# Kernel tuning notes

Measured on AMD Instinct MI355X. Metric: run time of the kernel, lower is better.

Reference implementation:

```python
import jax, jax.numpy as jnp
import numpy as np

N = 200000
D_NODE = 256
D_EDGE = 128
D_OUT = 256
J = 17


def setup_inputs() -> dict:
    key = jax.random.key(0)
    ks = jax.random.split(key, 16)
    s = 0.02
    return {
        "nodes_1": jax.random.normal(ks[0], (N, D_NODE), jnp.float32),
        "nodes_2": jax.random.normal(ks[1], (N, D_NODE), jnp.float32),
        "edges": jax.random.normal(ks[2], (N, D_EDGE), jnp.float32),
        "node_types_1": jax.random.randint(ks[3], (N,), 0, J),
        "node_types_2": jax.random.randint(ks[4], (N,), 0, J),
        # per-joint linear stacks (torch Linear weight [out,in] stored transposed as [in,out])
        "W1": jax.random.normal(ks[5], (J, D_NODE, D_OUT), jnp.float32) * s,
        "b1": jax.random.normal(ks[6], (J, D_OUT), jnp.float32) * s,
        "W2": jax.random.normal(ks[7], (J, D_NODE, D_OUT), jnp.float32) * s,
        "b2": jax.random.normal(ks[8], (J, D_OUT), jnp.float32) * s,
        "We": jax.random.normal(ks[9], (D_EDGE, D_OUT), jnp.float32) * s,
        "be": jax.random.normal(ks[10], (D_OUT,), jnp.float32) * s,
        "Wout": jax.random.normal(ks[11], (3 * D_OUT, D_OUT), jnp.float32) * s,
        "bout": jax.random.normal(ks[12], (D_OUT,), jnp.float32) * s,
    }


def _per_type_linear(nodes, types, W, b):
    # Equivalent to: for each joint i, tmp[types==i] = nodes[types==i] @ W[i] + b[i]
    out = jnp.zeros((nodes.shape[0], W.shape[2]), nodes.dtype)
    for i in range(W.shape[0]):  # small fixed loop over joint types
        yi = nodes @ W[i] + b[i]
        out = jnp.where((types == i)[:, None], yi, out)
    return out


def reference(nodes_1, nodes_2, edges, node_types_1, node_types_2,
              W1, b1, W2, b2, We, be, Wout, bout):
    tmp_1 = _per_type_linear(nodes_1, node_types_1, W1, b1)
    tmp_2 = _per_type_linear(nodes_2, node_types_2, W2, b2)
    e = edges @ We + be
    cat = jnp.concatenate([tmp_1, tmp_2, e], axis=1)  # [N, 3*D_OUT]
    h = jax.nn.relu(cat) @ Wout + bout
    return jax.nn.relu(h)
```

## Files before the change

kernel.cpp:

```cpp
#include <hip/hip_runtime.h>


#define J_TYPES 17
#define PAIRS   (J_TYPES * J_TYPES)
#define DN      256
#define DE      128
#define DO      256
#define TILE    64
#define LDA     264
#define LDE     136

typedef short bf16x8 __attribute__((ext_vector_type(8)));
typedef float f32x4  __attribute__((ext_vector_type(4)));

#define BAR() asm volatile("s_waitcnt lgkmcnt(0)\n\ts_barrier" ::: "memory")

__device__ __forceinline__ unsigned short f2bf(float x) {
  unsigned u = __float_as_uint(x);
  return (unsigned short)((u + 0x7fffu + ((u >> 16) & 1u)) >> 16);
}

__device__ __forceinline__ unsigned cvtpk(float lo, float hi) {
  unsigned r;
  asm("v_cvt_pk_bf16_f32 %0, %1, %2" : "=v"(r) : "v"(lo), "v"(hi));
  return r;
}

__global__ void prep_w_k(const float* __restrict__ W1, const float* __restrict__ W2,
                         const float* __restrict__ We, const float* __restrict__ Wout,
                         unsigned short* __restrict__ W1t, unsigned short* __restrict__ W2t,
                         unsigned short* __restrict__ Wet, unsigned short* __restrict__ Ut) {
  const int SZW = J_TYPES * 65536;
  const int total = SZW * 2 + DE * DO + 3 * 65536;
  for (int o = blockIdx.x * blockDim.x + threadIdx.x; o < total;
       o += gridDim.x * blockDim.x) {
    int idx = o;
    if (idx < SZW) {
      int j = idx >> 16, r = idx & 65535;
      int i = r & 7, lane = (r >> 3) & 63, t = r >> 9;
      int k32 = t & 7, colt = t >> 3;
      int col = colt * 16 + (lane & 15);
      int k = k32 * 32 + ((lane >> 4) << 3) + i;
      W1t[idx] = f2bf(W1[((size_t)j * 256 + k) * 256 + col]);
    } else if ((idx -= SZW) < SZW) {
      int j = idx >> 16, r = idx & 65535;
      int i = r & 7, lane = (r >> 3) & 63, t = r >> 9;
      int k32 = t & 7, colt = t >> 3;
      int col = colt * 16 + (lane & 15);
      int k = k32 * 32 + ((lane >> 4) << 3) + i;
      W2t[idx] = f2bf(W2[((size_t)j * 256 + k) * 256 + col]);
    } else if ((idx -= SZW) < DE * DO) {
      int r = idx;
      int i = r & 7, lane = (r >> 3) & 63, t = r >> 9;
      int k32 = t & 3, colt = t >> 2;
      int col = colt * 16 + (lane & 15);
      int k = k32 * 32 + ((lane >> 4) << 3) + i;
      Wet[idx] = f2bf(We[(size_t)k * 256 + col]);
    } else {
      idx -= DE * DO;
      int p = idx >> 16, r = idx & 65535;
      int i = r & 7, lane = (r >> 3) & 63, t = r >> 9;
      int k32 = t & 7, colt = t >> 3;
      int col = colt * 16 + (lane & 15);
      int k = k32 * 32 + ((lane >> 4) << 3) + i;
      Ut[idx] = f2bf(Wout[((size_t)p * 256 + k) * 256 + col]);
    }
  }
}

__global__ void hist_k(const int* __restrict__ ty1, const int* __restrict__ ty2,
                       int* __restrict__ cnt, int N) {
  __shared__ int h[PAIRS];
  for (int i = threadIdx.x; i < PAIRS; i += blockDim.x) h[i] = 0;
  __syncthreads();
  for (int i = blockIdx.x * blockDim.x + threadIdx.x; i < N;
       i += gridDim.x * blockDim.x)
    atomicAdd(&h[ty1[i] * J_TYPES + ty2[i]], 1);
  __syncthreads();
  for (int i = threadIdx.x; i < PAIRS; i += blockDim.x) {
    int v = h[i];
    if (v) atomicAdd(&cnt[i], v);
  }
}

__global__ void scan_tiles_k(const int* __restrict__ cnt, int* __restrict__ seg,
                             int* __restrict__ tpair, int* __restrict__ tstart,
                             int* __restrict__ tnr, int* __restrict__ ntl) {
  __shared__ int s1[512], s2[512];
  int t = threadIdx.x;
  int c  = (t < PAIRS) ? cnt[t] : 0;
  int nt = (c + TILE - 1) / TILE;
  s1[t] = c; s2[t] = nt;
  __syncthreads();
  for (int o = 1; o < 512; o <<= 1) {
    int v1 = (t >= o) ? s1[t - o] : 0;
    int v2 = (t >= o) ? s2[t - o] : 0;
    __syncthreads();
    s1[t] += v1; s2[t] += v2;
    __syncthreads();
  }
  if (t < PAIRS) {
    int segstart = s1[t] - c;
    int tbase    = s2[t] - nt;
    seg[t] = segstart;
    for (int i = 0; i < nt; ++i) {
      tpair[tbase + i]  = t;
      tstart[tbase + i] = segstart + i * TILE;
      int rem = c - i * TILE;
      tnr[tbase + i] = rem < TILE ? rem : TILE;
    }
  }
  if (t == 511) ntl[0] = s2[511];
}

__global__ void scatter_k(const int* __restrict__ ty1, const int* __restrict__ ty2,
                          const int* __restrict__ seg, int* __restrict__ c2,
                          int* __restrict__ ridx, int N) {
  __shared__ int lh[PAIRS], lb[PAIRS];
  int chunk = (N + gridDim.x - 1) / gridDim.x;
  int lo = blockIdx.x * chunk;
  int hi = lo + chunk; if (hi > N) hi = N;
  for (int i = threadIdx.x; i < PAIRS; i += blockDim.x) lh[i] = 0;
  __syncthreads();
  for (int i = lo + threadIdx.x; i < hi; i += blockDim.x)
    atomicAdd(&lh[ty1[i] * J_TYPES + ty2[i]], 1);
  __syncthreads();
  for (int i = threadIdx.x; i < PAIRS; i += blockDim.x) {
    int v = lh[i];
    lb[i] = v ? atomicAdd(&c2[i], v) : 0;
    lh[i] = 0;
  }
  __syncthreads();
  for (int i = lo + threadIdx.x; i < hi; i += blockDim.x) {
    int p = ty1[i] * J_TYPES + ty2[i];
    int pos = seg[p] + lb[p] + atomicAdd(&lh[p], 1);
    ridx[pos] = i;
  }
}


__device__ __forceinline__ void stage_issue256(const float* __restrict__ src,
                                               const int* __restrict__ ridxp, int nrows,
                                               int wave, int lane, float4 f[16]) {
#pragma unroll
  for (int j = 0; j < 16; ++j) {
    int r = wave + 4 * j;
    int rc = r < nrows ? r : nrows - 1;
    int sr = ridxp[rc];
    f[j] = reinterpret_cast<const float4*>(src + (size_t)sr * DN)[lane];
  }
}

__device__ __forceinline__ void stage_write256(const float4 f[16],
                                               unsigned short* lds, int wave, int lane) {
#pragma unroll
  for (int j = 0; j < 16; ++j) {
    int r = wave + 4 * j;
    unsigned lo = cvtpk(f[j].x, f[j].y), hi = cvtpk(f[j].z, f[j].w);
    *reinterpret_cast<uint2*>(lds + r * LDA + lane * 4) = make_uint2(lo, hi);
  }
}

__device__ __forceinline__ void stage_issue128(const float* __restrict__ src,
                                               const int* __restrict__ ridxp, int nrows,
                                               int wave, int lane, float2 f[16]) {
#pragma unroll
  for (int j = 0; j < 16; ++j) {
    int r = wave + 4 * j;
    int rc = r < nrows ? r : nrows - 1;
    int sr = ridxp[rc];
    f[j] = reinterpret_cast<const float2*>(src + (size_t)sr * DE)[lane];
  }
}

__device__ __forceinline__ void stage_write128(const float2 f[16],
                                               unsigned short* lds, int wave, int lane) {
#pragma unroll
  for (int j = 0; j < 16; ++j) {
    int r = wave + 4 * j;
    *reinterpret_cast<unsigned*>(lds + r * LDE + lane * 2) = cvtpk(f[j].x, f[j].y);
  }
}

template <int NK, int LD>
__device__ __forceinline__ void gemm_full(const unsigned short* lds,
                                          const unsigned short* __restrict__ Wbase,
                                          f32x4 acc[4][4], int r0, int kg, int lane,
                                          int wave) {
  const unsigned short* w = Wbase + ((size_t)(wave * 4) * NK) * 512 + lane * 8;
  bf16x8 bf[2][4];
#pragma unroll
  for (int cs = 0; cs < 4; ++cs)
    bf[0][cs] = *reinterpret_cast<const bf16x8*>(w + ((size_t)cs * NK) * 512);
#pragma unroll
  for (int k32 = 0; k32 < NK; ++k32) {
    const int cur = k32 & 1, nxt = cur ^ 1;
    if (k32 + 1 < NK) {
#pragma unroll
      for (int cs = 0; cs < 4; ++cs)
        bf[nxt][cs] =
            *reinterpret_cast<const bf16x8*>(w + ((size_t)cs * NK + k32 + 1) * 512);
    }
    bf16x8 af[4];
#pragma unroll
    for (int rs = 0; rs < 4; ++rs)
      af[rs] = *reinterpret_cast<const bf16x8*>(lds + (rs * 16 + r0) * LD + k32 * 32 + kg);
    __builtin_amdgcn_s_setprio(1);
#pragma unroll
    for (int rs = 0; rs < 4; ++rs)
#pragma unroll
      for (int cs = 0; cs < 4; ++cs)
        acc[rs][cs] = __builtin_amdgcn_mfma_f32_16x16x32_bf16(af[rs], bf[cur][cs],
                                                              acc[rs][cs], 0, 0, 0);
    __builtin_amdgcn_s_setprio(0);
  }
}

__device__ __forceinline__ void epi_full(f32x4 accT[4][4], const float* __restrict__ bias,
                                         unsigned short* ldsT, int r0, int rb, int wave) {
#pragma unroll
  for (int cs = 0; cs < 4; ++cs) {
    int col = wave * 64 + cs * 16 + r0;
    float b = bias[col];
#pragma unroll
    for (int rs = 0; rs < 4; ++rs) {
      float x0 = fmaxf(accT[rs][cs][0] + b, 0.f);
      float x1 = fmaxf(accT[rs][cs][1] + b, 0.f);
      float x2 = fmaxf(accT[rs][cs][2] + b, 0.f);
      float x3 = fmaxf(accT[rs][cs][3] + b, 0.f);
      unsigned w01 = cvtpk(x0, x1), w23 = cvtpk(x2, x3);
      int row = rs * 16 + rb;
      ldsT[(row + 0) * LDA + col] = (unsigned short)w01;
      ldsT[(row + 1) * LDA + col] = (unsigned short)(w01 >> 16);
      ldsT[(row + 2) * LDA + col] = (unsigned short)w23;
      ldsT[(row + 3) * LDA + col] = (unsigned short)(w23 >> 16);
    }
  }
}

#define ZERO44(A)                      \
  _Pragma("unroll") for (int a_ = 0; a_ < 4; ++a_) _Pragma("unroll") \
      for (int b_ = 0; b_ < 4; ++b_) A[a_][b_] = (f32x4){0.f, 0.f, 0.f, 0.f};

__global__ __launch_bounds__(256, 2) void fused_k(
    const float* __restrict__ n1, const float* __restrict__ n2,
    const float* __restrict__ eg, const unsigned short* __restrict__ W1t,
    const unsigned short* __restrict__ W2t, const unsigned short* __restrict__ Wet,
    const unsigned short* __restrict__ Ut, const float* __restrict__ b1,
    const float* __restrict__ b2, const float* __restrict__ be,
    const float* __restrict__ bout, const int* __restrict__ ridx,
    const int* __restrict__ tpair, const int* __restrict__ tstart,
    const int* __restrict__ tnr, const int* __restrict__ ntl,
    float* __restrict__ out) {
  int nwg = gridDim.x, orig = blockIdx.x;
  int q = nwg >> 3, rr = nwg & 7, xc = orig & 7, sidx = orig >> 3;
  int tile = (xc < rr ? xc * (q + 1) : rr * (q + 1) + (xc - rr) * q) + sidx;
  if (tile >= ntl[0]) return;

  const int pr = tpair[tile];
  const int t1 = pr / J_TYPES, t2 = pr % J_TYPES;
  const int ts = tstart[tile];
  const int nrows = tnr[tile];
  const int* __restrict__ ridxp = ridx + ts;

  __shared__ unsigned short ldsA[TILE * LDA];
  __shared__ unsigned short ldsT[TILE * LDA];
  __shared__ int srow[TILE];

  const int lane = threadIdx.x & 63;
  const int wave = __builtin_amdgcn_readfirstlane(threadIdx.x >> 6);
  const int r0 = lane & 15;
  const int kg = (lane >> 4) * 8;
  const int rb = (lane >> 4) * 4;

  if (threadIdx.x < TILE)
    srow[threadIdx.x] = (threadIdx.x < nrows) ? ridxp[threadIdx.x] : -1;

  f32x4 accT[4][4], accO[4][4];
  float4 s4[16];
  float2 s2[16];

  stage_issue256(n1, ridxp, nrows, wave, lane, s4);
  stage_write256(s4, ldsA, wave, lane);
  BAR();

  stage_issue256(n2, ridxp, nrows, wave, lane, s4);
  ZERO44(accT);
  gemm_full<8, LDA>(ldsA, W1t + (size_t)t1 * 65536, accT, r0, kg, lane, wave);
  BAR();

  epi_full(accT, b1 + t1 * 256, ldsT, r0, rb, wave);
  stage_write256(s4, ldsA, wave, lane);
  BAR();

  stage_issue128(eg, ridxp, nrows, wave, lane, s2);
  ZERO44(accO);
  gemm_full<8, LDA>(ldsT, Ut, accO, r0, kg, lane, wave);
  ZERO44(accT);
  gemm_full<8, LDA>(ldsA, W2t + (size_t)t2 * 65536, accT, r0, kg, lane, wave);
  BAR();

  epi_full(accT, b2 + t2 * 256, ldsT, r0, rb, wave);
  stage_write128(s2, ldsA, wave, lane);
  BAR();

  gemm_full<8, LDA>(ldsT, Ut + 65536, accO, r0, kg, lane, wave);
  ZERO44(accT);
  gemm_full<4, LDE>(ldsA, Wet, accT, r0, kg, lane, wave);
  BAR();

  epi_full(accT, be, ldsT, r0, rb, wave);
  BAR();

  gemm_full<8, LDA>(ldsT, Ut + 2 * 65536, accO, r0, kg, lane, wave);

#pragma unroll
  for (int cs = 0; cs < 4; ++cs) {
    int col = wave * 64 + cs * 16 + r0;
    float bo = bout[col];
#pragma unroll
    for (int rs = 0; rs < 4; ++rs)
#pragma unroll
      for (int i = 0; i < 4; ++i) {
        int row = rs * 16 + rb + i;
        if (row < nrows) {
          float v = fmaxf(accO[rs][cs][i] + bo, 0.f);
          out[(size_t)srow[row] * 256 + col] = v;
        }
      }
  }
}

extern "C" void kernel_launch(void* const* d_in, const int* in_sizes, int n_in,
                              void* d_out, int out_size, void* d_ws, size_t ws_size,
                              hipStream_t stream) {
  const float* n1   = (const float*)d_in[0];
  const float* n2   = (const float*)d_in[1];
  const float* eg   = (const float*)d_in[2];
  const int*   ty1  = (const int*)d_in[3];
  const int*   ty2  = (const int*)d_in[4];
  const float* W1   = (const float*)d_in[5];
  const float* b1   = (const float*)d_in[6];
  const float* W2   = (const float*)d_in[7];
  const float* b2   = (const float*)d_in[8];
  const float* We   = (const float*)d_in[9];
  const float* be   = (const float*)d_in[10];
  const float* Wout = (const float*)d_in[11];
  const float* bout = (const float*)d_in[12];
  float* out = (float*)d_out;

  const int N = in_sizes[0] / DN;
  const int maxt = (N + TILE - 1) / TILE + PAIRS;

  char* ws = (char*)d_ws;
  size_t off = 0;
  auto take = [&](size_t bytes) -> char* {
    char* p = ws + off;
    off += (bytes + 255) & ~(size_t)255;
    return p;
  };
  int* cnt = (int*)take(PAIRS * 4);
  int* c2  = (int*)take(PAIRS * 4);
  int* ntl = (int*)take(4);
  int* seg = (int*)take((PAIRS + 1) * 4);
  int* tp  = (int*)take((size_t)maxt * 4);
  int* tst = (int*)take((size_t)maxt * 4);
  int* tnr = (int*)take((size_t)maxt * 4);
  int* ridx = (int*)take((size_t)N * 4);
  unsigned short* W1t = (unsigned short*)take((size_t)J_TYPES * 65536 * 2);
  unsigned short* W2t = (unsigned short*)take((size_t)J_TYPES * 65536 * 2);
  unsigned short* Wet = (unsigned short*)take((size_t)DE * DO * 2);
  unsigned short* Ut  = (unsigned short*)take((size_t)3 * 65536 * 2);
  (void)ws_size; (void)n_in; (void)out_size;

  hipMemsetAsync(cnt, 0, (size_t)((char*)seg - (char*)cnt), stream);
  prep_w_k<<<1024, 256, 0, stream>>>(W1, W2, We, Wout, W1t, W2t, Wet, Ut);
  hist_k<<<400, 256, 0, stream>>>(ty1, ty2, cnt, N);
  scan_tiles_k<<<1, 512, 0, stream>>>(cnt, seg, tp, tst, tnr, ntl);
  scatter_k<<<256, 256, 0, stream>>>(ty1, ty2, seg, c2, ridx, N);
  fused_k<<<maxt, 256, 0, stream>>>(n1, n2, eg, W1t, W2t, Wet, Ut, b1, b2, be, bout,
                                    ridx, tp, tst, tnr, ntl, out);
}
```

Baseline: 323.1 us.

## Split fused kernel across eight waves with 32-column slices and rotated K order

The fused per-tile kernel moves from 4 waves of 64 output columns to 8 waves of 32 columns each, halving accumulator and staging register use per thread. The launch bound goes to 512 threads with a higher occupancy target. Staging no longer holds loads in registers across a GEMM to prefetch; each stage now loads and writes to LDS in one step. The K loop start is rotated per wave to spread LDS bank accesses. This trades away the load/compute overlap in exchange for more waves per CU to hide latency.

```diff
diff --git a/kernel.cpp b/kernel.cpp
--- a/kernel.cpp
+++ b/kernel.cpp
@@ -139,88 +139,85 @@
 }
 
 
-__device__ __forceinline__ void stage_issue256(const float* __restrict__ src,
-                                               const int* __restrict__ ridxp, int nrows,
-                                               int wave, int lane, float4 f[16]) {
-#pragma unroll
-  for (int j = 0; j < 16; ++j) {
-    int r = wave + 4 * j;
+__device__ __forceinline__ void stage256(const float* __restrict__ src,
+                                         const int* __restrict__ ridxp, int nrows,
+                                         unsigned short* lds, int wave, int lane) {
+  float4 f[8];
+#pragma unroll
+  for (int j = 0; j < 8; ++j) {
+    int r = wave + 8 * j;
     int rc = r < nrows ? r : nrows - 1;
     int sr = ridxp[rc];
     f[j] = reinterpret_cast<const float4*>(src + (size_t)sr * DN)[lane];
   }
-}
-
-__device__ __forceinline__ void stage_write256(const float4 f[16],
-                                               unsigned short* lds, int wave, int lane) {
-#pragma unroll
-  for (int j = 0; j < 16; ++j) {
-    int r = wave + 4 * j;
+#pragma unroll
+  for (int j = 0; j < 8; ++j) {
+    int r = wave + 8 * j;
     unsigned lo = cvtpk(f[j].x, f[j].y), hi = cvtpk(f[j].z, f[j].w);
     *reinterpret_cast<uint2*>(lds + r * LDA + lane * 4) = make_uint2(lo, hi);
   }
 }
 
-__device__ __forceinline__ void stage_issue128(const float* __restrict__ src,
-                                               const int* __restrict__ ridxp, int nrows,
-                                               int wave, int lane, float2 f[16]) {
-#pragma unroll
-  for (int j = 0; j < 16; ++j) {
-    int r = wave + 4 * j;
+__device__ __forceinline__ void stage128(const float* __restrict__ src,
+                                         const int* __restrict__ ridxp, int nrows,
+                                         unsigned short* lds, int wave, int lane) {
+  float2 f[8];
+#pragma unroll
+  for (int j = 0; j < 8; ++j) {
+    int r = wave + 8 * j;
     int rc = r < nrows ? r : nrows - 1;
     int sr = ridxp[rc];
     f[j] = reinterpret_cast<const float2*>(src + (size_t)sr * DE)[lane];
   }
-}
-
-__device__ __forceinline__ void stage_write128(const float2 f[16],
-                                               unsigned short* lds, int wave, int lane) {
-#pragma unroll
-  for (int j = 0; j < 16; ++j) {
-    int r = wave + 4 * j;
+#pragma unroll
+  for (int j = 0; j < 8; ++j) {
+    int r = wave + 8 * j;
     *reinterpret_cast<unsigned*>(lds + r * LDE + lane * 2) = cvtpk(f[j].x, f[j].y);
   }
 }
 
 template <int NK, int LD>
-__device__ __forceinline__ void gemm_full(const unsigned short* lds,
-                                          const unsigned short* __restrict__ Wbase,
-                                          f32x4 acc[4][4], int r0, int kg, int lane,
-                                          int wave) {
-  const unsigned short* w = Wbase + ((size_t)(wave * 4) * NK) * 512 + lane * 8;
-  bf16x8 bf[2][4];
-#pragma unroll
-  for (int cs = 0; cs < 4; ++cs)
-    bf[0][cs] = *reinterpret_cast<const bf16x8*>(w + ((size_t)cs * NK) * 512);
-#pragma unroll
-  for (int k32 = 0; k32 < NK; ++k32) {
-    const int cur = k32 & 1, nxt = cur ^ 1;
-    if (k32 + 1 < NK) {
-#pragma unroll
-      for (int cs = 0; cs < 4; ++cs)
+__device__ __forceinline__ void gemm32(const unsigned short* lds,
+                                       const unsigned short* __restrict__ Wbase,
+                                       f32x4 acc[4][2], int r0, int kg, int lane,
+                                       int wave) {
+  const unsigned short* w = Wbase + ((size_t)(wave * 2) * NK) * 512 + lane * 8;
+  const int kw = wave & (NK - 1);
+  bf16x8 bf[2][2];
+#pragma unroll
+  for (int cs = 0; cs < 2; ++cs)
+    bf[0][cs] = *reinterpret_cast<const bf16x8*>(w + ((size_t)cs * NK + kw) * 512);
+#pragma unroll
+  for (int i = 0; i < NK; ++i) {
+    const int cur = i & 1, nxt = cur ^ 1;
+    const int kk = (i + wave) & (NK - 1);
+    if (i + 1 < NK) {
+      const int kk1 = (i + 1 + wave) & (NK - 1);
+#pragma unroll
+      for (int cs = 0; cs < 2; ++cs)
         bf[nxt][cs] =
-            *reinterpret_cast<const bf16x8*>(w + ((size_t)cs * NK + k32 + 1) * 512);
+            *reinterpret_cast<const bf16x8*>(w + ((size_t)cs * NK + kk1) * 512);
     }
     bf16x8 af[4];
 #pragma unroll
     for (int rs = 0; rs < 4; ++rs)
-      af[rs] = *reinterpret_cast<const bf16x8*>(lds + (rs * 16 + r0) * LD + k32 * 32 + kg);
+      af[rs] = *reinterpret_cast<const bf16x8*>(lds + (rs * 16 + r0) * LD + kk * 32 + kg);
     __builtin_amdgcn_s_setprio(1);
 #pragma unroll
     for (int rs = 0; rs < 4; ++rs)
 #pragma unroll
-      for (int cs = 0; cs < 4; ++cs)
+      for (int cs = 0; cs < 2; ++cs)
         acc[rs][cs] = __builtin_amdgcn_mfma_f32_16x16x32_bf16(af[rs], bf[cur][cs],
                                                               acc[rs][cs], 0, 0, 0);
     __builtin_amdgcn_s_setprio(0);
   }
 }
 
-__device__ __forceinline__ void epi_full(f32x4 accT[4][4], const float* __restrict__ bias,
-                                         unsigned short* ldsT, int r0, int rb, int wave) {
-#pragma unroll
-  for (int cs = 0; cs < 4; ++cs) {
-    int col = wave * 64 + cs * 16 + r0;
+__device__ __forceinline__ void epi32(f32x4 accT[4][2], const float* __restrict__ bias,
+                                      unsigned short* ldsT, int r0, int rb, int wave) {
+#pragma unroll
+  for (int cs = 0; cs < 2; ++cs) {
+    int col = wave * 32 + cs * 16 + r0;
     float b = bias[col];
 #pragma unroll
     for (int rs = 0; rs < 4; ++rs) {
@@ -238,11 +235,11 @@
   }
 }
 
-#define ZERO44(A)                      \
-  _Pragma("unroll") for (int a_ = 0; a_ < 4; ++a_) _Pragma("unroll") \
-      for (int b_ = 0; b_ < 4; ++b_) A[a_][b_] = (f32x4){0.f, 0.f, 0.f, 0.f};
-
-__global__ __launch_bounds__(256, 2) void fused_k(
+#define ZERO42(A)                                                        \
+  _Pragma("unroll") for (int a_ = 0; a_ < 4; ++a_) _Pragma("unroll")     \
+      for (int b_ = 0; b_ < 2; ++b_) A[a_][b_] = (f32x4){0.f, 0.f, 0.f, 0.f};
+
+__global__ __launch_bounds__(512, 4) void fused_k(
     const float* __restrict__ n1, const float* __restrict__ n2,
     const float* __restrict__ eg, const unsigned short* __restrict__ W1t,
     const unsigned short* __restrict__ W2t, const unsigned short* __restrict__ Wet,
@@ -276,47 +273,42 @@
   if (threadIdx.x < TILE)
     srow[threadIdx.x] = (threadIdx.x < nrows) ? ridxp[threadIdx.x] : -1;
 
-  f32x4 accT[4][4], accO[4][4];
-  float4 s4[16];
-  float2 s2[16];
-
-  stage_issue256(n1, ridxp, nrows, wave, lane, s4);
-  stage_write256(s4, ldsA, wave, lane);
-  BAR();
-
-  stage_issue256(n2, ridxp, nrows, wave, lane, s4);
-  ZERO44(accT);
-  gemm_full<8, LDA>(ldsA, W1t + (size_t)t1 * 65536, accT, r0, kg, lane, wave);
-  BAR();
-
-  epi_full(accT, b1 + t1 * 256, ldsT, r0, rb, wave);
-  stage_write256(s4, ldsA, wave, lane);
-  BAR();
-
-  stage_issue128(eg, ridxp, nrows, wave, lane, s2);
-  ZERO44(accO);
-  gemm_full<8, LDA>(ldsT, Ut, accO, r0, kg, lane, wave);
-  ZERO44(accT);
-  gemm_full<8, LDA>(ldsA, W2t + (size_t)t2 * 65536, accT, r0, kg, lane, wave);
-  BAR();
-
-  epi_full(accT, b2 + t2 * 256, ldsT, r0, rb, wave);
-  stage_write128(s2, ldsA, wave, lane);
-  BAR();
-
-  gemm_full<8, LDA>(ldsT, Ut + 65536, accO, r0, kg, lane, wave);
-  ZERO44(accT);
-  gemm_full<4, LDE>(ldsA, Wet, accT, r0, kg, lane, wave);
-  BAR();
-
-  epi_full(accT, be, ldsT, r0, rb, wave);
-  BAR();
-
-  gemm_full<8, LDA>(ldsT, Ut + 2 * 65536, accO, r0, kg, lane, wave);
-
-#pragma unroll
-  for (int cs = 0; cs < 4; ++cs) {
-    int col = wave * 64 + cs * 16 + r0;
+  f32x4 accT[4][2], accO[4][2];
+
+  stage256(n1, ridxp, nrows, ldsA, wave, lane);
+  BAR();
+
+  ZERO42(accT);
+  gemm32<8, LDA>(ldsA, W1t + (size_t)t1 * 65536, accT, r0, kg, lane, wave);
+  BAR();
+
+  epi32(accT, b1 + t1 * 256, ldsT, r0, rb, wave);
+  stage256(n2, ridxp, nrows, ldsA, wave, lane);
+  BAR();
+
+  ZERO42(accO);
+  gemm32<8, LDA>(ldsT, Ut, accO, r0, kg, lane, wave);
+  ZERO42(accT);
+  gemm32<8, LDA>(ldsA, W2t + (size_t)t2 * 65536, accT, r0, kg, lane, wave);
+  BAR();
+
+  epi32(accT, b2 + t2 * 256, ldsT, r0, rb, wave);
+  stage128(eg, ridxp, nrows, ldsA, wave, lane);
+  BAR();
+
+  gemm32<8, LDA>(ldsT, Ut + 65536, accO, r0, kg, lane, wave);
+  ZERO42(accT);
+  gemm32<4, LDE>(ldsA, Wet, accT, r0, kg, lane, wave);
+  BAR();
+
+  epi32(accT, be, ldsT, r0, rb, wave);
+  BAR();
+
+  gemm32<8, LDA>(ldsT, Ut + 2 * 65536, accO, r0, kg, lane, wave);
+
+#pragma unroll
+  for (int cs = 0; cs < 2; ++cs) {
+    int col = wave * 32 + cs * 16 + r0;
     float bo = bout[col];
 #pragma unroll
     for (int rs = 0; rs < 4; ++rs)
@@ -378,6 +370,6 @@
   hist_k<<<400, 256, 0, stream>>>(ty1, ty2, cnt, N);
   scan_tiles_k<<<1, 512, 0, stream>>>(cnt, seg, tp, tst, tnr, ntl);
   scatter_k<<<256, 256, 0, stream>>>(ty1, ty2, seg, c2, ridx, N);
-  fused_k<<<maxt, 256, 0, stream>>>(n1, n2, eg, W1t, W2t, Wet, Ut, b1, b2, be, bout,
+  fused_k<<<maxt, 512, 0, stream>>>(n1, n2, eg, W1t, W2t, Wet, Ut, b1, b2, be, bout,
                                     ridx, tp, tst, tnr, ntl, out);
 }
```

Measured after the change: 289.5 us (median of 3 runs). 1.12x faster.
